# Kernel optimization log

Measured on AMD Instinct MI355X. Metric: run time of the kernel, lower is better.

## Reference

```python
import jax, jax.numpy as jnp
import numpy as np

# dims
M = 64      # memory_num -> T after attention pooling
B = 16
T = 2048    # input sequence length
C = 1024    # dim
H = 16      # attention heads
G = 2       # groups
V = 320     # num_vars
VQ = 1024   # vq_dim
D = VQ // G # var_dim = 512
TAU = 2.0   # curr_temp = max_temp at step 0


def setup_inputs() -> dict:
    key = jax.random.key(0)
    ks = jax.random.split(key, 16)
    s = 1.0 / np.sqrt(C)
    x = jax.random.normal(ks[0], (T, B, C), jnp.float32)
    padding_mask = jnp.zeros((B, T), bool)
    memory = jax.random.uniform(ks[1], (M, 1, C), jnp.float32)
    Wq = jax.random.normal(ks[2], (C, C), jnp.float32) * s
    Wk = jax.random.normal(ks[3], (C, C), jnp.float32) * s
    Wv = jax.random.normal(ks[4], (C, C), jnp.float32) * s
    Wo = jax.random.normal(ks[5], (C, C), jnp.float32) * s
    bq = jnp.zeros((C,), jnp.float32)
    bk = jnp.zeros((C,), jnp.float32)
    bv = jnp.zeros((C,), jnp.float32)
    bo = jnp.zeros((C,), jnp.float32)
    Wp = jax.random.normal(ks[6], (G * V, C), jnp.float32) * s
    bp = jnp.zeros((G * V,), jnp.float32)
    codebook = jax.random.uniform(ks[7], (1, G * V, D), jnp.float32)
    u = jax.random.uniform(ks[8], (B * M, G * V), jnp.float32, 1e-6, 1.0 - 1e-6)
    gumbel = -jnp.log(-jnp.log(u))
    return {"x": x, "padding_mask": padding_mask, "gumbel": gumbel,
            "memory": memory, "Wq": Wq, "bq": bq, "Wk": Wk, "bk": bk,
            "Wv": Wv, "bv": bv, "Wo": Wo, "bo": bo, "Wp": Wp, "bp": bp,
            "codebook": codebook}


def reference(x, padding_mask, gumbel, memory, Wq, bq, Wk, bk, Wv, bv, Wo, bo, Wp, bp, codebook):
    hd = C // H
    scale = hd ** -0.5
    # --- memory attention: queries are M learned memory slots, keys/values = x ---
    q = jnp.broadcast_to(memory, (M, B, C))              # repeat(1, B, 1)
    q = (q @ Wq.T + bq) * scale                          # [M,B,C]
    k = x @ Wk.T + bk                                    # [T,B,C]
    v = x @ Wv.T + bv
    split = lambda t: t.reshape(t.shape[0], B, H, hd).transpose(1, 2, 0, 3)  # [B,H,len,hd]
    qh, kh, vh = split(q), split(k), split(v)
    scores = jnp.einsum('bhqd,bhkd->bhqk', qh, kh)       # [B,H,M,T]
    neg = jnp.finfo(scores.dtype).min
    scores = jnp.where(padding_mask[:, None, None, :], neg, scores)
    attn = jax.nn.softmax(scores, axis=-1)
    ctx = jnp.einsum('bhqk,bhkd->bhqd', attn, vh)        # [B,H,M,hd]
    ctx = ctx.transpose(2, 0, 1, 3).reshape(M, B, C)
    h = ctx @ Wo.T + bo                                  # [M,B,C]
    # --- vector quantization (gumbel-softmax, hard=True, straight-through) ---
    h = h.transpose(1, 0, 2).reshape(B * M, C)           # [BT, C]
    logits = h @ Wp.T + bp                               # [BT, G*V]
    lg = logits.reshape(B * M * G, V)
    y = jax.nn.softmax((lg + gumbel.reshape(B * M * G, V)) / TAU, axis=-1)
    hard = jax.nn.one_hot(jnp.argmax(y, axis=-1), V, dtype=y.dtype)
    st = hard + y - jax.lax.stop_gradient(y)             # straight-through one-hot
    sel = st.reshape(B * M, G, V)
    code = codebook.reshape(G, V, D)
    # onehot-multiply-sum expressed as contraction (same math, no [BT,G*V,D] blowup)
    out = jnp.einsum('ngv,gvd->ngd', sel, code).reshape(B, M, G * D)
    out = out.transpose(1, 0, 2)                         # [T_mem, B, vq_dim]
    vq_logits = jax.nn.softmax(logits.reshape(B * M, G, V), axis=-1)
    return out, vq_logits
```

## Files before the change

### kernel.cpp

```cpp
#include <hip/hip_runtime.h>
#include <hip/hip_bf16.h>
#include <cstdint>
#include <cstddef>

#define TM 2048
#define BB 16
#define CC 1024
#define HH 16
#define HD 64
#define MM 64
#define GG 2
#define VV 320
#define DD 512

typedef __attribute__((ext_vector_type(4))) float f32x4;
typedef __attribute__((ext_vector_type(8))) short s16x8;
typedef __attribute__((ext_vector_type(8))) unsigned short u16x8;
typedef __attribute__((ext_vector_type(4))) unsigned int u32x4;

#define SW4(r) ((((r) & 3) ^ (((r) >> 2) & 3)))

#define GLL16(gp, lp) __builtin_amdgcn_global_load_lds( \
    (const __attribute__((address_space(1))) unsigned int*)(gp), \
    (__attribute__((address_space(3))) unsigned int*)(lp), 16, 0, 0)

static __device__ __forceinline__ unsigned short bf16_rne(float f) {
    unsigned u = __builtin_bit_cast(unsigned, f);
    u += 0x7FFFu + ((u >> 16) & 1u);
    return (unsigned short)(u >> 16);
}
static __device__ __forceinline__ float bf16_f32(unsigned short b) {
    return __builtin_bit_cast(float, (unsigned)b << 16);
}

__global__ void wsplit_swz(const float* __restrict__ W,
                           unsigned short* __restrict__ hi,
                           unsigned short* __restrict__ lo, int ngroups) {
    int gidx = blockIdx.x * 256 + threadIdx.x;
    if (gidx >= ngroups) return;
    int row = gidx >> 7;
    int sl  = gidx & 127;
    int k   = sl * 8;
    int slot = (k >> 3) & 3;
    int kp = (k & ~31) | (((slot ^ SW4(row & 15)) & 3) << 3);
    const float* src = W + (size_t)row * 1024 + k;
    f32x4 a = *(const f32x4*)src;
    f32x4 b = *(const f32x4*)(src + 4);
    u16x8 h, l;
    #pragma unroll
    for (int e = 0; e < 4; ++e) {
        unsigned short hh = bf16_rne(a[e]); h[e] = hh; l[e] = bf16_rne(a[e] - bf16_f32(hh));
        unsigned short hh2 = bf16_rne(b[e]); h[4 + e] = hh2; l[4 + e] = bf16_rne(b[e] - bf16_f32(hh2));
    }
    *(u16x8*)(hi + (size_t)row * 1024 + kp) = h;
    *(u16x8*)(lo + (size_t)row * 1024 + kp) = l;
}

__global__ __launch_bounds__(256) void gemm_f32_64(
    const float* __restrict__ A, const float* __restrict__ W,
    const float* __restrict__ bias, float* __restrict__ C,
    int K, int N, float alpha)
{
    __shared__ float At[64][17];
    __shared__ float Wt[64][17];
    const int tid = threadIdx.x;
    const int tx = tid & 15, ty = tid >> 4;
    const int n0 = blockIdx.x * 64, r0 = blockIdx.y * 64;
    const int srow = tid >> 2, skc = (tid & 3) * 4;

    float acc[4][4] = {};
    const float* ap = A + (size_t)(r0 + srow) * K + skc;
    const float* wp = W + (size_t)(n0 + srow) * K + skc;

    for (int k0 = 0; k0 < K; k0 += 16) {
        f32x4 av = *(const f32x4*)(ap + k0);
        f32x4 wv = *(const f32x4*)(wp + k0);
        __syncthreads();
        #pragma unroll
        for (int e = 0; e < 4; ++e) { At[srow][skc + e] = av[e]; Wt[srow][skc + e] = wv[e]; }
        __syncthreads();
        #pragma unroll
        for (int k = 0; k < 16; ++k) {
            float a[4], b[4];
            #pragma unroll
            for (int i = 0; i < 4; ++i) a[i] = At[ty + 16 * i][k];
            #pragma unroll
            for (int j = 0; j < 4; ++j) b[j] = Wt[tx + 16 * j][k];
            #pragma unroll
            for (int i = 0; i < 4; ++i)
                #pragma unroll
                for (int j = 0; j < 4; ++j)
                    acc[i][j] += a[i] * b[j];
        }
    }
    float bv[4];
    #pragma unroll
    for (int j = 0; j < 4; ++j) bv[j] = bias[n0 + tx + 16 * j];
    #pragma unroll
    for (int i = 0; i < 4; ++i)
        #pragma unroll
        for (int j = 0; j < 4; ++j)
            C[(size_t)(r0 + ty + 16 * i) * N + (n0 + tx + 16 * j)] = (acc[i][j] + bv[j]) * alpha;
}

__global__ __launch_bounds__(256) void kv_gemm3(
    const unsigned short* __restrict__ Xh, const unsigned short* __restrict__ Xl,
    const unsigned short* __restrict__ WKh, const unsigned short* __restrict__ WKl,
    const unsigned short* __restrict__ WVh, const unsigned short* __restrict__ WVl,
    const float* __restrict__ biasK, const float* __restrict__ biasV,
    unsigned short* __restrict__ outK, unsigned short* __restrict__ outV)
{
    const unsigned short* Wh; const unsigned short* Wl; const float* bias; unsigned short* out;
    if (blockIdx.z == 0) { Wh = WKh; Wl = WKl; bias = biasK; out = outK; }
    else                 { Wh = WVh; Wl = WVl; bias = biasV; out = outV; }

    const int rb = blockIdx.x * 32 + (blockIdx.y >> 3);
    const int cb = blockIdx.y & 7;
    const int r0 = rb * 128, n0 = cb * 128;

    __shared__ unsigned short Ah[128 * 32];
    __shared__ unsigned short Al[128 * 32];
    __shared__ unsigned short Bh[128 * 32];
    __shared__ unsigned short Bl[128 * 32];

    const int tid = threadIdx.x;
    const int lane = tid & 63;
    const int w = tid >> 6;
    const int wr = w >> 1, wc = w & 1;
    const int l15 = lane & 15;
    const int g = lane >> 4;
    const int lrow = lane >> 2;
    const int lslot = lane & 3;
    const int w32 = w * 32;

    f32x4 acc[4][4];
    #pragma unroll
    for (int i = 0; i < 4; ++i)
        #pragma unroll
        for (int j = 0; j < 4; ++j) acc[i][j] = f32x4{0.f, 0.f, 0.f, 0.f};

    for (int k0 = 0; k0 < CC; k0 += 32) {
        __syncthreads();
        #pragma unroll
        for (int i = 0; i < 2; ++i) {
            const int rs = w32 + i * 16;
            const size_t ga = (size_t)(r0 + rs + lrow) * CC + k0 + lslot * 8;
            const size_t gb = (size_t)(n0 + rs + lrow) * CC + k0 + lslot * 8;
            GLL16(Xh + ga, &Ah[rs * 32]);
            GLL16(Xl + ga, &Al[rs * 32]);
            GLL16(Wh + gb, &Bh[rs * 32]);
            GLL16(Wl + gb, &Bl[rs * 32]);
        }
        __syncthreads();

        s16x8 bhf[4], blf[4];
        #pragma unroll
        for (int ni = 0; ni < 4; ++ni) {
            int col = wc * 64 + ni * 16 + l15;
            int off = col * 32 + (((g ^ SW4(col & 15)) & 3) << 3);
            bhf[ni] = *(const s16x8*)&Bh[off];
            blf[ni] = *(const s16x8*)&Bl[off];
        }
        #pragma unroll
        for (int mi = 0; mi < 4; ++mi) {
            int row = wr * 64 + mi * 16 + l15;
            int off = row * 32 + (((g ^ SW4(row & 15)) & 3) << 3);
            s16x8 ah = *(const s16x8*)&Ah[off];
            s16x8 al = *(const s16x8*)&Al[off];
            #pragma unroll
            for (int ni = 0; ni < 4; ++ni) {
                acc[mi][ni] = __builtin_amdgcn_mfma_f32_16x16x32_bf16(ah, bhf[ni], acc[mi][ni], 0, 0, 0);
                acc[mi][ni] = __builtin_amdgcn_mfma_f32_16x16x32_bf16(al, bhf[ni], acc[mi][ni], 0, 0, 0);
                acc[mi][ni] = __builtin_amdgcn_mfma_f32_16x16x32_bf16(ah, blf[ni], acc[mi][ni], 0, 0, 0);
            }
        }
    }

    #pragma unroll
    for (int ni = 0; ni < 4; ++ni) {
        int col = n0 + wc * 64 + ni * 16 + l15;
        float bv = bias[col];
        int hh = col >> 6, d = col & 63;
        #pragma unroll
        for (int mi = 0; mi < 4; ++mi) {
            #pragma unroll
            for (int j = 0; j < 4; ++j) {
                int r = r0 + wr * 64 + mi * 16 + g * 4 + j;
                int t = r >> 4, bb = r & 15;
                size_t base = ((size_t)(bb * HH + hh) * TM + t) * 128;
                float val = acc[mi][ni][j] + bv;
                unsigned short hi = bf16_rne(val);
                out[base + d] = hi;
                out[base + 64 + d] = bf16_rne(val - bf16_f32(hi));
            }
        }
    }
}

__global__ __launch_bounds__(256) void kv_gemm2(
    const float* __restrict__ X,
    const unsigned short* __restrict__ WKh, const unsigned short* __restrict__ WKl,
    const unsigned short* __restrict__ WVh, const unsigned short* __restrict__ WVl,
    const float* __restrict__ biasK, const float* __restrict__ biasV,
    unsigned short* __restrict__ outK, unsigned short* __restrict__ outV)
{
    const unsigned short* Wh; const unsigned short* Wl; const float* bias; unsigned short* out;
    if (blockIdx.z == 0) { Wh = WKh; Wl = WKl; bias = biasK; out = outK; }
    else                 { Wh = WVh; Wl = WVl; bias = biasV; out = outV; }

    const int rb = blockIdx.x * 32 + (blockIdx.y >> 3);
    const int cb = blockIdx.y & 7;
    const int r0 = rb * 128, n0 = cb * 128;

    __shared__ unsigned short Ah[128 * 32];
    __shared__ unsigned short Al[128 * 32];
    __shared__ unsigned short Bh[128 * 32];
    __shared__ unsigned short Bl[128 * 32];

    const int tid = threadIdx.x;
    const int lane = tid & 63;
    const int wid = tid >> 6;
    const int wr = wid >> 1, wc = wid & 1;
    const int l15 = lane & 15;
    const int g = lane >> 4;

    f32x4 acc[4][4];
    #pragma unroll
    for (int i = 0; i < 4; ++i)
        #pragma unroll
        for (int j = 0; j < 4; ++j) acc[i][j] = f32x4{0.f, 0.f, 0.f, 0.f};

    for (int k0 = 0; k0 < CC; k0 += 32) {
        f32x4 xa[2][2]; u16x8 wbh[2], wbl[2];
        int rowc[2], slotc[2];
        #pragma unroll
        for (int c = 0; c < 2; ++c) {
            int g2 = tid + 256 * c;
            int row = g2 >> 2, slot = g2 & 3;
            rowc[c] = row; slotc[c] = slot;
            const float* xp = X + (size_t)(r0 + row) * CC + k0 + slot * 8;
            xa[c][0] = *(const f32x4*)xp;
            xa[c][1] = *(const f32x4*)(xp + 4);
            wbh[c] = *(const u16x8*)(Wh + (size_t)(n0 + row) * CC + k0 + slot * 8);
            wbl[c] = *(const u16x8*)(Wl + (size_t)(n0 + row) * CC + k0 + slot * 8);
        }
        __syncthreads();
        #pragma unroll
        for (int c = 0; c < 2; ++c) {
            int row = rowc[c], slot = slotc[c];
// ... 316 lines not shown
                unsigned g0 = __shfl(pkl[2 * ks][0], srcB), g1 = __shfl(pkl[2 * ks + 1][0], srcB);
                tl[2] = hsel ? g1 : g0;
                unsigned h0 = __shfl(pkl[2 * ks][1], srcB), h1 = __shfl(pkl[2 * ks + 1][1], srcB);
                tl[3] = hsel ? h1 : h0;
            }
            Ph[ks] = __builtin_bit_cast(s16x8, th);
            Pl[ks] = __builtin_bit_cast(s16x8, tl);
        }

        #pragma unroll
        for (int mt = 0; mt < 4; ++mt) {
            int dr = mt * 16 + l15;
            #pragma unroll
            for (int ks = 0; ks < 2; ++ks) {
                int spb = ((ks * 4 + g) ^ (dr & 7)) & 7;
                s16x8 vh = *(const s16x8*)&Vt[buf][dr * 128 + spb * 8];
                s16x8 vl = *(const s16x8*)&Vt[buf][dr * 128 + (8 + spb) * 8];
                O[mt] = __builtin_amdgcn_mfma_f32_16x16x32_bf16(vh, Ph[ks], O[mt], 0, 0, 0);
                O[mt] = __builtin_amdgcn_mfma_f32_16x16x32_bf16(vl, Ph[ks], O[mt], 0, 0, 0);
                O[mt] = __builtin_amdgcn_mfma_f32_16x16x32_bf16(vh, Pl[ks], O[mt], 0, 0, 0);
            }
        }

        __syncthreads();
        if (ch + 1 < NCH) { WRITE_LDS(buf ^ 1); }
        __syncthreads();
    }

    const int qg = w * 16 + l15;
    if (SPLIT == 1) {
        float inv = 1.0f / l_run;
        #pragma unroll
        for (int mt = 0; mt < 4; ++mt)
            #pragma unroll
            for (int j = 0; j < 4; ++j) {
                int d = mt * 16 + g * 4 + j;
                ctx_or_pO[(size_t)(b * MM + qg) * CC + h * 64 + d] = O[mt][j] * inv;
            }
    } else {
        float* po = ctx_or_pO + (size_t)bid * 4096;
        #pragma unroll
        for (int mt = 0; mt < 4; ++mt)
            #pragma unroll
            for (int j = 0; j < 4; ++j) {
                int d = mt * 16 + g * 4 + j;
                po[d * 64 + qg] = O[mt][j];
            }
        if (g == 0) { partM[bid * 64 + qg] = m_run; partL[bid * 64 + qg] = l_run; }
    }
    #undef ISSUE_LOADS
    #undef WRITE_LDS
}

__global__ __launch_bounds__(256) void attn_merge(
    const float* __restrict__ pO, const float* __restrict__ pM,
    const float* __restrict__ pL, float* __restrict__ ctx)
{
    const int bh = blockIdx.x, b = bh >> 4, h = bh & 15, tid = threadIdx.x;
    __shared__ float w0s[64], w1s[64], invs[64];
    if (tid < 64) {
        float m0 = pM[(bh * 2) * 64 + tid], m1 = pM[(bh * 2 + 1) * 64 + tid];
        float l0 = pL[(bh * 2) * 64 + tid], l1 = pL[(bh * 2 + 1) * 64 + tid];
        float M = fmaxf(m0, m1);
        float w0 = expf(m0 - M), w1 = expf(m1 - M);
        w0s[tid] = w0; w1s[tid] = w1;
        invs[tid] = 1.0f / (l0 * w0 + l1 * w1);
    }
    __syncthreads();
    const float* o0 = pO + (size_t)(bh * 2) * 4096;
    const float* o1 = pO + (size_t)(bh * 2 + 1) * 4096;
    #pragma unroll
    for (int i = 0; i < 16; ++i) {
        int e = tid + 256 * i;
        int q = e >> 6, d = e & 63;
        float v = o0[d * 64 + q] * w0s[q] + o1[d * 64 + q] * w1s[q];
        ctx[(size_t)(b * MM + q) * CC + h * 64 + d] = v * invs[q];
    }
}

__global__ __launch_bounds__(256) void finalize_kernel(
    const float* __restrict__ logits, const float* __restrict__ gumbel,
    const float* __restrict__ codebook, float* __restrict__ out)
{
    __shared__ float lrow[GG * VV];
    __shared__ float red[256];
    __shared__ int redi[256];
    __shared__ int sel[GG];

    const int n = blockIdx.x, tid = threadIdx.x;
    const size_t OUT1 = (size_t)MM * BB * GG * DD;

    for (int e = tid; e < GG * VV; e += 256) lrow[e] = logits[(size_t)n * GG * VV + e];
    __syncthreads();

    for (int g = 0; g < GG; ++g) {
        float bvv = -3.0e38f; int bii = 0x7FFFFFFF;
        for (int j = tid; j < VV; j += 256) {
            float z = lrow[g * VV + j] + gumbel[(size_t)n * GG * VV + g * VV + j];
            if (z > bvv) { bvv = z; bii = j; }
        }
        red[tid] = bvv; redi[tid] = bii;
        __syncthreads();
        for (int s = 128; s > 0; s >>= 1) {
            if (tid < s) {
                float ov = red[tid + s]; int oi = redi[tid + s];
                if (ov > red[tid] || (ov == red[tid] && oi < redi[tid])) { red[tid] = ov; redi[tid] = oi; }
            }
            __syncthreads();
        }
        if (tid == 0) sel[g] = redi[0];
        __syncthreads();

        float mx = -3.0e38f;
        for (int j = tid; j < VV; j += 256) mx = fmaxf(mx, lrow[g * VV + j]);
        red[tid] = mx;
        __syncthreads();
        for (int s = 128; s > 0; s >>= 1) {
            if (tid < s) red[tid] = fmaxf(red[tid], red[tid + s]);
            __syncthreads();
        }
        float rmax = red[0];
        __syncthreads();
        float sm = 0.f;
        for (int j = tid; j < VV; j += 256) sm += expf(lrow[g * VV + j] - rmax);
        red[tid] = sm;
        __syncthreads();
        for (int s = 128; s > 0; s >>= 1) {
            if (tid < s) red[tid] += red[tid + s];
            __syncthreads();
// ... 8 lines not shown
    const int b = n >> 6, m = n & 63;
    const size_t ob = ((size_t)m * BB + b) * (GG * DD);
    for (int g = 0; g < GG; ++g) {
        const float* cb = codebook + ((size_t)g * VV + sel[g]) * DD;
        for (int d = tid; d < DD; d += 256) out[ob + g * DD + d] = cb[d];
    }
}

extern "C" void kernel_launch(void* const* d_in, const int* in_sizes, int n_in,
                              void* d_out, int out_size, void* d_ws, size_t ws_size,
                              hipStream_t stream)
{
    const float* x        = (const float*)d_in[0];
    const float* gumbel   = (const float*)d_in[2];
    const float* memory   = (const float*)d_in[3];
    const float* Wq       = (const float*)d_in[4];
    const float* bq       = (const float*)d_in[5];
    const float* Wk       = (const float*)d_in[6];
    const float* bk       = (const float*)d_in[7];
    const float* Wv       = (const float*)d_in[8];
    const float* bv       = (const float*)d_in[9];
    const float* Wo       = (const float*)d_in[10];
    const float* bo       = (const float*)d_in[11];
    const float* Wp       = (const float*)d_in[12];
    const float* bp       = (const float*)d_in[13];
    const float* codebook = (const float*)d_in[14];
    float* out = (float*)d_out;

    char* ws = (char*)d_ws;
    size_t off = 0;
    auto take = [&](size_t bytes) -> void* {
        void* p = ws + off;
        off = (off + bytes + 255) & ~(size_t)255;
        return p;
    };

    float* q_ws   = (float*)take((size_t)MM * CC * 4);
    float* ctx_ws = (float*)take((size_t)BB * MM * CC * 4);
    float* lg_ws  = (float*)take((size_t)BB * MM * GG * VV * 4);
    unsigned short* wkh = (unsigned short*)take((size_t)CC * CC * 2);
    unsigned short* wkl = (unsigned short*)take((size_t)CC * CC * 2);
    unsigned short* wvh = (unsigned short*)take((size_t)CC * CC * 2);
    unsigned short* wvl = (unsigned short*)take((size_t)CC * CC * 2);
    unsigned short* k_ws = (unsigned short*)take((size_t)BB * HH * TM * 128 * 2);
    unsigned short* v_ws = (unsigned short*)take((size_t)BB * HH * TM * 128 * 2);

    const size_t XROWS = (size_t)TM * BB;
    const size_t xplane = XROWS * CC * 2;
    const size_t extra_need = 2 * (size_t)CC * CC * 2
                            + 2 * (size_t)GG * VV * CC * 2
                            + 2 * xplane + (1u << 20);
    const bool newpath = (ws_size >= off + extra_need);

    {
        int ngroups = CC * (CC / 8);
        wsplit_swz<<<dim3((ngroups + 255) / 256), 256, 0, stream>>>(Wk, wkh, wkl, ngroups);
        wsplit_swz<<<dim3((ngroups + 255) / 256), 256, 0, stream>>>(Wv, wvh, wvl, ngroups);
    }
    gemm_f32_64<<<dim3(CC / 64, MM / 64), 256, 0, stream>>>(memory, Wq, bq, q_ws, CC, CC, 0.125f);

    if (newpath) {
        unsigned short* woh = (unsigned short*)take((size_t)CC * CC * 2);
        unsigned short* wol = (unsigned short*)take((size_t)CC * CC * 2);
        unsigned short* wph = (unsigned short*)take((size_t)GG * VV * CC * 2);
        unsigned short* wpl = (unsigned short*)take((size_t)GG * VV * CC * 2);
        unsigned short* xh  = (unsigned short*)take(xplane);
        unsigned short* xl  = (unsigned short*)take(xplane);

        char* xr = (char*)xh;
        size_t xo = 0;
        auto xtake = [&](size_t bytes) -> void* {
            void* p = xr + xo;
            xo = (xo + bytes + 255) & ~(size_t)255;
            return p;
        };
        float* pO = (float*)xtake((size_t)512 * 4096 * 4);
        float* pM = (float*)xtake((size_t)512 * 64 * 4);
        float* pL = (float*)xtake((size_t)512 * 64 * 4);
        unsigned short* cth = (unsigned short*)xtake((size_t)BB * MM * CC * 2);
        unsigned short* ctl = (unsigned short*)xtake((size_t)BB * MM * CC * 2);
        unsigned short* hh  = (unsigned short*)xtake((size_t)BB * MM * CC * 2);
        unsigned short* hl  = (unsigned short*)xtake((size_t)BB * MM * CC * 2);

        {
            int ngroups = CC * (CC / 8);
            wsplit_swz<<<dim3((ngroups + 255) / 256), 256, 0, stream>>>(Wo, woh, wol, ngroups);
            int ngp = GG * VV * (CC / 8);
            wsplit_swz<<<dim3((ngp + 255) / 256), 256, 0, stream>>>(Wp, wph, wpl, ngp);
            int ngx = (int)(XROWS * (CC / 8));
            wsplit_swz<<<dim3((ngx + 255) / 256), 256, 0, stream>>>(x, xh, xl, ngx);
        }

        kv_gemm3<<<dim3(8, 256, 2), 256, 0, stream>>>(xh, xl, wkh, wkl, wvh, wvl, bk, bv, k_ws, v_ws);

        attn2<2><<<dim3(512), 256, 0, stream>>>(q_ws, k_ws, v_ws, pO, pM, pL);
        attn_merge<<<dim3(256), 256, 0, stream>>>(pO, pM, pL, ctx_ws);

        {
            int ngc = BB * MM * (CC / 8);
            wsplit_swz<<<dim3((ngc + 255) / 256), 256, 0, stream>>>(ctx_ws, cth, ctl, ngc);
        }
        mfma_gemm3<1><<<dim3(CC / 128, (BB * MM) / 128), 256, 0, stream>>>(
            cth, ctl, woh, wol, bo, CC, nullptr, hh, hl);
        mfma_gemm3<0><<<dim3((GG * VV) / 128, (BB * MM) / 128), 256, 0, stream>>>(
            hh, hl, wph, wpl, bp, GG * VV, lg_ws, nullptr, nullptr);
    } else {
        float* h_ws = (float*)take((size_t)BB * MM * CC * 4);
        const size_t part_bytes = (size_t)512 * 4096 * 4 + 2 * (size_t)512 * 64 * 4 + 4096;
        const bool split2 = (ws_size >= off + part_bytes);

        kv_gemm2<<<dim3(8, 256, 2), 256, 0, stream>>>(x, wkh, wkl, wvh, wvl, bk, bv, k_ws, v_ws);

        if (split2) {
            float* pO = (float*)take((size_t)512 * 4096 * 4);
            float* pM = (float*)take((size_t)512 * 64 * 4);
            float* pL = (float*)take((size_t)512 * 64 * 4);
            attn2<2><<<dim3(512), 256, 0, stream>>>(q_ws, k_ws, v_ws, pO, pM, pL);
            attn_merge<<<dim3(256), 256, 0, stream>>>(pO, pM, pL, ctx_ws);
        } else {
            attn2<1><<<dim3(256), 256, 0, stream>>>(q_ws, k_ws, v_ws, ctx_ws, nullptr, nullptr);
        }

        gemm_f32_64<<<dim3(CC / 64, (BB * MM) / 64), 256, 0, stream>>>(ctx_ws, Wo, bo, h_ws, CC, CC, 1.0f);
        gemm_f32_64<<<dim3((GG * VV) / 64, (BB * MM) / 64), 256, 0, stream>>>(h_ws, Wp, bp, lg_ws, CC, GG * VV, 1.0f);
    }

    finalize_kernel<<<dim3(BB * MM), 256, 0, stream>>>(lg_ws, gumbel, codebook, out);
}
```

Measured before the change: 802.2 us.

## Rework K/V projection GEMM with 512 threads, triple-buffered LDS and staged epilogue

Replaces the K/V projection GEMM with a 512-thread variant. Each of the 8 warps now covers a 64x32 sub-tile, and the single-buffer global-to-LDS loop becomes a 3-stage pipeline with explicit vmcnt waits and raised MFMA priority, so loads overlap compute. The epilogue writes the bf16 hi/lo outputs through a swizzled LDS tile and then stores 16-byte vectors, replacing scattered 2-byte global stores. This uses three times the LDS (96KB), which can reduce occupancy, and fewer accumulators per warp means more LDS reads per MFMA.

```diff
diff --git a/kernel.cpp b/kernel.cpp
--- a/kernel.cpp
+++ b/kernel.cpp
@@ -103,7 +103,7 @@
             C[(size_t)(r0 + ty + 16 * i) * N + (n0 + tx + 16 * j)] = (acc[i][j] + bv[j]) * alpha;
 }
 
-__global__ __launch_bounds__(256) void kv_gemm3(
+__global__ __launch_bounds__(512) void kv_gemm4(
     const unsigned short* __restrict__ Xh, const unsigned short* __restrict__ Xl,
     const unsigned short* __restrict__ WKh, const unsigned short* __restrict__ WKl,
     const unsigned short* __restrict__ WVh, const unsigned short* __restrict__ WVl,
@@ -118,81 +118,126 @@
     const int cb = blockIdx.y & 7;
     const int r0 = rb * 128, n0 = cb * 128;
 
-    __shared__ unsigned short Ah[128 * 32];
-    __shared__ unsigned short Al[128 * 32];
-    __shared__ unsigned short Bh[128 * 32];
-    __shared__ unsigned short Bl[128 * 32];
+    __shared__ unsigned short L[3][4][128 * 32];
 
     const int tid = threadIdx.x;
     const int lane = tid & 63;
     const int w = tid >> 6;
-    const int wr = w >> 1, wc = w & 1;
+    const int wr = w >> 2, wc = w & 3;
     const int l15 = lane & 15;
     const int g = lane >> 4;
-    const int lrow = lane >> 2;
-    const int lslot = lane & 3;
-    const int w32 = w * 32;
-
-    f32x4 acc[4][4];
+    const int srow = tid >> 2;
+    const int sslot = tid & 3;
+    const int w512 = w * 512;
+
+    const size_t gaBase = (size_t)(r0 + srow) * CC + sslot * 8;
+    const size_t gbBase = (size_t)(n0 + srow) * CC + sslot * 8;
+
+    #define STAGE4(buf, k0)                                   \
+        {                                                     \
+            GLL16(Xh + gaBase + (k0), &L[buf][0][w512]);      \
+            GLL16(Xl + gaBase + (k0), &L[buf][1][w512]);      \
+            GLL16(Wh + gbBase + (k0), &L[buf][2][w512]);      \
+            GLL16(Wl + gbBase + (k0), &L[buf][3][w512]);      \
+        }
+
+    f32x4 acc[4][2];
     #pragma unroll
     for (int i = 0; i < 4; ++i)
         #pragma unroll
-        for (int j = 0; j < 4; ++j) acc[i][j] = f32x4{0.f, 0.f, 0.f, 0.f};
-
-    for (int k0 = 0; k0 < CC; k0 += 32) {
-        __syncthreads();
-        #pragma unroll
-        for (int i = 0; i < 2; ++i) {
-            const int rs = w32 + i * 16;
-            const size_t ga = (size_t)(r0 + rs + lrow) * CC + k0 + lslot * 8;
-            const size_t gb = (size_t)(n0 + rs + lrow) * CC + k0 + lslot * 8;
-            GLL16(Xh + ga, &Ah[rs * 32]);
-            GLL16(Xl + ga, &Al[rs * 32]);
-            GLL16(Wh + gb, &Bh[rs * 32]);
-            GLL16(Wl + gb, &Bl[rs * 32]);
-        }
-        __syncthreads();
-
-        s16x8 bhf[4], blf[4];
-        #pragma unroll
-        for (int ni = 0; ni < 4; ++ni) {
-            int col = wc * 64 + ni * 16 + l15;
-            int off = col * 32 + (((g ^ SW4(col & 15)) & 3) << 3);
-            bhf[ni] = *(const s16x8*)&Bh[off];
-            blf[ni] = *(const s16x8*)&Bl[off];
-        }
+        for (int j = 0; j < 2; ++j) acc[i][j] = f32x4{0.f, 0.f, 0.f, 0.f};
+
+    int aoff[4], boff[2];
+    #pragma unroll
+    for (int mi = 0; mi < 4; ++mi) {
+        int row = wr * 64 + mi * 16 + l15;
+        aoff[mi] = row * 32 + (((g ^ SW4(row & 15)) & 3) << 3);
+    }
+    #pragma unroll
+    for (int ni = 0; ni < 2; ++ni) {
+        int col = wc * 32 + ni * 16 + l15;
+        boff[ni] = col * 32 + (((g ^ SW4(col & 15)) & 3) << 3);
+    }
+
+    STAGE4(0, 0);
+    STAGE4(1, 32);
+    asm volatile("s_waitcnt vmcnt(4)" ::: "memory");
+    __builtin_amdgcn_s_barrier();
+
+    const int NT = 32;
+    for (int t = 0; t < NT; ++t) {
+        const int buf = t % 3;
+        if (t + 2 < NT) {
+            const int stg = (t + 2) % 3;
+            STAGE4(stg, (t + 2) * 32);
+        }
+
+        s16x8 bhf[2], blf[2];
+        #pragma unroll
+        for (int ni = 0; ni < 2; ++ni) {
+            bhf[ni] = *(const s16x8*)&L[buf][2][boff[ni]];
+            blf[ni] = *(const s16x8*)&L[buf][3][boff[ni]];
+        }
+        s16x8 ah[4], al[4];
         #pragma unroll
         for (int mi = 0; mi < 4; ++mi) {
-            int row = wr * 64 + mi * 16 + l15;
-            int off = row * 32 + (((g ^ SW4(row & 15)) & 3) << 3);
-            s16x8 ah = *(const s16x8*)&Ah[off];
-            s16x8 al = *(const s16x8*)&Al[off];
-            #pragma unroll
-            for (int ni = 0; ni < 4; ++ni) {
-                acc[mi][ni] = __builtin_amdgcn_mfma_f32_16x16x32_bf16(ah, bhf[ni], acc[mi][ni], 0, 0, 0);
-                acc[mi][ni] = __builtin_amdgcn_mfma_f32_16x16x32_bf16(al, bhf[ni], acc[mi][ni], 0, 0, 0);
-                acc[mi][ni] = __builtin_amdgcn_mfma_f32_16x16x32_bf16(ah, blf[ni], acc[mi][ni], 0, 0, 0);
-            }
-        }
-    }
-
-    #pragma unroll
-    for (int ni = 0; ni < 4; ++ni) {
-        int col = n0 + wc * 64 + ni * 16 + l15;
-        float bv = bias[col];
-        int hh = col >> 6, d = col & 63;
+            ah[mi] = *(const s16x8*)&L[buf][0][aoff[mi]];
+            al[mi] = *(const s16x8*)&L[buf][1][aoff[mi]];
+        }
+
+        __builtin_amdgcn_s_setprio(1);
         #pragma unroll
         for (int mi = 0; mi < 4; ++mi) {
             #pragma unroll
+            for (int ni = 0; ni < 2; ++ni) {
+                acc[mi][ni] = __builtin_amdgcn_mfma_f32_16x16x32_bf16(ah[mi], bhf[ni], acc[mi][ni], 0, 0, 0);
+                acc[mi][ni] = __builtin_amdgcn_mfma_f32_16x16x32_bf16(al[mi], bhf[ni], acc[mi][ni], 0, 0, 0);
+                acc[mi][ni] = __builtin_amdgcn_mfma_f32_16x16x32_bf16(ah[mi], blf[ni], acc[mi][ni], 0, 0, 0);
+            }
+        }
+        __builtin_amdgcn_s_setprio(0);
+
+        if (t + 2 < NT) {
+            asm volatile("s_waitcnt vmcnt(4)" ::: "memory");
+        } else if (t + 1 < NT) {
+            asm volatile("s_waitcnt vmcnt(0)" ::: "memory");
+        }
+        __builtin_amdgcn_s_barrier();
+    }
+    #undef STAGE4
+
+    __syncthreads();
+    unsigned short* OutL = &L[0][0][0];
+    #pragma unroll
+    for (int ni = 0; ni < 2; ++ni) {
+        const int cl = wc * 32 + ni * 16 + l15;
+        const float bv = bias[n0 + cl];
+        const int hsel = cl >> 6, d = cl & 63;
+        const int qh = (hsel << 4) + (d >> 3), ql = qh + 8;
+        #pragma unroll
+        for (int mi = 0; mi < 4; ++mi) {
+            #pragma unroll
             for (int j = 0; j < 4; ++j) {
-                int r = r0 + wr * 64 + mi * 16 + g * 4 + j;
-                int t = r >> 4, bb = r & 15;
-                size_t base = ((size_t)(bb * HH + hh) * TM + t) * 128;
+                const int rl = wr * 64 + mi * 16 + g * 4 + j;
                 float val = acc[mi][ni][j] + bv;
                 unsigned short hi = bf16_rne(val);
-                out[base + d] = hi;
-                out[base + 64 + d] = bf16_rne(val - bf16_f32(hi));
-            }
+                OutL[rl * 256 + ((qh ^ (rl & 31)) << 3) + (d & 7)] = hi;
+                OutL[rl * 256 + ((ql ^ (rl & 31)) << 3) + (d & 7)] = bf16_rne(val - bf16_f32(hi));
+            }
+        }
+    }
+    __syncthreads();
+    {
+        const int r = tid >> 2;
+        const int hsel2 = (tid >> 1) & 1, c2 = tid & 1;
+        const int rg = r0 + r;
+        const int tt = rg >> 4, bb2 = rg & 15;
+        const int hh2 = (n0 >> 6) + hsel2;
+        unsigned short* dst = out + ((size_t)(bb2 * HH + hh2) * TM + tt) * 128 + c2 * 64;
+        #pragma unroll
+        for (int i2 = 0; i2 < 8; ++i2) {
+            const int q = (hsel2 << 4) + (c2 << 3) + i2;
+            *(u16x8*)(dst + i2 * 8) = *(const u16x8*)&OutL[r * 256 + ((q ^ (r & 31)) << 3)];
         }
     }
 }
@@ -793,7 +838,7 @@
             wsplit_swz<<<dim3((ngx + 255) / 256), 256, 0, stream>>>(x, xh, xl, ngx);
         }
 
-        kv_gemm3<<<dim3(8, 256, 2), 256, 0, stream>>>(xh, xl, wkh, wkl, wvh, wvl, bk, bv, k_ws, v_ws);
+        kv_gemm4<<<dim3(8, 256, 2), 512, 0, stream>>>(xh, xl, wkh, wkl, wvh, wvl, bk, bv, k_ws, v_ws);
 
         attn2<2><<<dim3(512), 256, 0, stream>>>(q_ws, k_ws, v_ws, pO, pM, pL);
         attn_merge<<<dim3(256), 256, 0, stream>>>(pO, pM, pL, ctx_ws);
```

After: 843.8 us. 5.2% more time.

## Replace K/V projection GEMM with 256x256-tile pipelined 512-thread MFMA kernel

Applied to the files above, without the earlier changes.

Replaces the 128x128-tile split-bf16 K/V GEMM with a 256x256-tile kernel of 8 waves. It double-buffers 64-wide K slabs loaded directly into LDS with an 8-way XOR swizzle, and treats the three hi/lo product terms as 48 sequential K tiles. It uses XCD-aware block mapping, s_setprio around MFMA bursts, and manual vmcnt waits. The epilogue stages results through LDS so the scattered per-head K/V stores become coalesced 16-byte writes. The aim is higher MFMA utilisation and less global traffic per FLOP, at the cost of one block per CU, many barriers, and fragile hand-tuned synchronisation.

```diff
diff --git a/kernel.cpp b/kernel.cpp
--- a/kernel.cpp
+++ b/kernel.cpp
@@ -39,10 +39,31 @@
     int gidx = blockIdx.x * 256 + threadIdx.x;
     if (gidx >= ngroups) return;
     int row = gidx >> 7;
-    int sl  = gidx & 127;
-    int k   = sl * 8;
+    int k   = (gidx & 127) * 8;
     int slot = (k >> 3) & 3;
     int kp = (k & ~31) | (((slot ^ SW4(row & 15)) & 3) << 3);
+    const float* src = W + (size_t)row * 1024 + k;
+    f32x4 a = *(const f32x4*)src;
+    f32x4 b = *(const f32x4*)(src + 4);
+    u16x8 h, l;
+    #pragma unroll
+    for (int e = 0; e < 4; ++e) {
+        unsigned short hh = bf16_rne(a[e]); h[e] = hh; l[e] = bf16_rne(a[e] - bf16_f32(hh));
+        unsigned short hh2 = bf16_rne(b[e]); h[4 + e] = hh2; l[4 + e] = bf16_rne(b[e] - bf16_f32(hh2));
+    }
+    *(u16x8*)(hi + (size_t)row * 1024 + kp) = h;
+    *(u16x8*)(lo + (size_t)row * 1024 + kp) = l;
+}
+
+__global__ void wsplit_swz8(const float* __restrict__ W,
+                            unsigned short* __restrict__ hi,
+                            unsigned short* __restrict__ lo, int ngroups) {
+    int gidx = blockIdx.x * 256 + threadIdx.x;
+    if (gidx >= ngroups) return;
+    int row = gidx >> 7;
+    int k   = (gidx & 127) * 8;
+    int slot = (k >> 3) & 7;
+    int kp = (k & ~63) | (((slot ^ (row & 7)) & 7) << 3);
     const float* src = W + (size_t)row * 1024 + k;
     f32x4 a = *(const f32x4*)src;
     f32x4 b = *(const f32x4*)(src + 4);
@@ -103,98 +124,165 @@
             C[(size_t)(r0 + ty + 16 * i) * N + (n0 + tx + 16 * j)] = (acc[i][j] + bv[j]) * alpha;
 }
 
-__global__ __launch_bounds__(256) void kv_gemm3(
+__global__ __launch_bounds__(512, 1) void kv_gemm8(
     const unsigned short* __restrict__ Xh, const unsigned short* __restrict__ Xl,
     const unsigned short* __restrict__ WKh, const unsigned short* __restrict__ WKl,
     const unsigned short* __restrict__ WVh, const unsigned short* __restrict__ WVl,
     const float* __restrict__ biasK, const float* __restrict__ biasV,
     unsigned short* __restrict__ outK, unsigned short* __restrict__ outV)
 {
-    const unsigned short* Wh; const unsigned short* Wl; const float* bias; unsigned short* out;
-    if (blockIdx.z == 0) { Wh = WKh; Wl = WKl; bias = biasK; out = outK; }
-    else                 { Wh = WVh; Wl = WVl; bias = biasV; out = outV; }
-
-    const int rb = blockIdx.x * 32 + (blockIdx.y >> 3);
-    const int cb = blockIdx.y & 7;
-    const int r0 = rb * 128, n0 = cb * 128;
-
-    __shared__ unsigned short Ah[128 * 32];
-    __shared__ unsigned short Al[128 * 32];
-    __shared__ unsigned short Bh[128 * 32];
-    __shared__ unsigned short Bl[128 * 32];
-
-    const int tid = threadIdx.x;
-    const int lane = tid & 63;
-    const int w = tid >> 6;
-    const int wr = w >> 1, wc = w & 1;
-    const int l15 = lane & 15;
-    const int g = lane >> 4;
-    const int lrow = lane >> 2;
-    const int lslot = lane & 3;
-    const int w32 = w * 32;
-
-    f32x4 acc[4][4];
-    #pragma unroll
-    for (int i = 0; i < 4; ++i)
-        #pragma unroll
-        for (int j = 0; j < 4; ++j) acc[i][j] = f32x4{0.f, 0.f, 0.f, 0.f};
-
-    for (int k0 = 0; k0 < CC; k0 += 32) {
-        __syncthreads();
-        #pragma unroll
-        for (int i = 0; i < 2; ++i) {
-            const int rs = w32 + i * 16;
-            const size_t ga = (size_t)(r0 + rs + lrow) * CC + k0 + lslot * 8;
-            const size_t gb = (size_t)(n0 + rs + lrow) * CC + k0 + lslot * 8;
-            GLL16(Xh + ga, &Ah[rs * 32]);
-            GLL16(Xl + ga, &Al[rs * 32]);
-            GLL16(Wh + gb, &Bh[rs * 32]);
-            GLL16(Wl + gb, &Bl[rs * 32]);
-        }
-        __syncthreads();
-
-        s16x8 bhf[4], blf[4];
-        #pragma unroll
-        for (int ni = 0; ni < 4; ++ni) {
-            int col = wc * 64 + ni * 16 + l15;
-            int off = col * 32 + (((g ^ SW4(col & 15)) & 3) << 3);
-            bhf[ni] = *(const s16x8*)&Bh[off];
-            blf[ni] = *(const s16x8*)&Bl[off];
-        }
-        #pragma unroll
-        for (int mi = 0; mi < 4; ++mi) {
-            int row = wr * 64 + mi * 16 + l15;
-            int off = row * 32 + (((g ^ SW4(row & 15)) & 3) << 3);
-            s16x8 ah = *(const s16x8*)&Ah[off];
-            s16x8 al = *(const s16x8*)&Al[off];
+    const int bid = blockIdx.x;
+    const int xcd = bid & 7, i = bid >> 3;
+    const int mb = xcd * 16 + (i >> 3);
+    const int j = i & 7, z = j >> 2, nb = j & 3;
+
+    const unsigned short *Bh_g, *Bl_g; const float* bias; unsigned short* out;
+    if (z == 0) { Bh_g = WKh; Bl_g = WKl; bias = biasK; out = outK; }
+    else        { Bh_g = WVh; Bl_g = WVl; bias = biasV; out = outV; }
+    const int r0 = mb * 256, n0 = nb * 256;
+
+    __shared__ __align__(16) unsigned short L[65536];
+
+    const int tid = threadIdx.x, lane = tid & 63, w = tid >> 6;
+    const int wr = w >> 2, wc = w & 3;
+    const int l15 = lane & 15, g = lane >> 4;
+
+    f32x4 acc[8][4];
+    #pragma unroll
+    for (int mi = 0; mi < 8; ++mi)
+        #pragma unroll
+        for (int ni = 0; ni < 4; ++ni) acc[mi][ni] = f32x4{0.f, 0.f, 0.f, 0.f};
+
+    auto STAGE_A = [&](int buf, int tau) {
+        const int k0in = (tau & 15) * 64;
+        const unsigned short* P = ((tau >> 4) == 1) ? Xl : Xh;
+        #pragma unroll
+        for (int half = 0; half < 2; ++half)
+            #pragma unroll
+            for (int ii = 0; ii < 2; ++ii) {
+                const int e0 = ii * 512 + w * 64;
+                const int e = e0 + lane;
+                const unsigned short* src = P + (size_t)(r0 + half * 128 + (e >> 3)) * 1024
+                                              + k0in + (e & 7) * 8;
+                GLL16(src, &L[(buf * 2 + half) * 8192 + e0 * 8]);
+            }
+    };
+    auto STAGE_B = [&](int buf, int tau) {
+        const int k0in = (tau & 15) * 64;
+        const unsigned short* P = ((tau >> 4) == 2) ? Bl_g : Bh_g;
+        #pragma unroll
+        for (int half = 0; half < 2; ++half)
+            #pragma unroll
+            for (int ii = 0; ii < 2; ++ii) {
+                const int e0 = ii * 512 + w * 64;
+                const int e = e0 + lane;
+                const unsigned short* src = P + (size_t)(n0 + half * 128 + (e >> 3)) * 1024
+                                              + k0in + (e & 7) * 8;
+                GLL16(src, &L[32768 + (buf * 2 + half) * 8192 + e0 * 8]);
+            }
+    };
+
+    s16x8 a_[8], b_[2];
+    #define RD_A(BUF, KS) { _Pragma("unroll")                                        \
+        for (int mi = 0; mi < 8; ++mi) {                                             \
+            int row = mi * 16 + l15;                                                 \
+            a_[mi] = *(const s16x8*)&L[((BUF) * 2 + wr) * 8192 + row * 64            \
+                                       + ((((KS) * 4 + g) ^ (l15 & 7)) << 3)]; } }
+    #define RD_B(BUF, KS, NF0) { _Pragma("unroll")                                   \
+        for (int q = 0; q < 2; ++q) {                                                \
+            int row = (wc & 1) * 64 + ((NF0) + q) * 16 + l15;                        \
+            b_[q] = *(const s16x8*)&L[32768 + ((BUF) * 2 + (wc >> 1)) * 8192         \
+                                      + row * 64 + ((((KS) * 4 + g) ^ (l15 & 7)) << 3)]; } }
+    #define MFMA16(NF0) { _Pragma("unroll")                                          \
+        for (int mi = 0; mi < 8; ++mi) {                                             \
+            acc[mi][NF0]     = __builtin_amdgcn_mfma_f32_16x16x32_bf16(a_[mi], b_[0], acc[mi][NF0], 0, 0, 0);     \
+            acc[mi][NF0 + 1] = __builtin_amdgcn_mfma_f32_16x16x32_bf16(a_[mi], b_[1], acc[mi][NF0 + 1], 0, 0, 0); } }
+    #define FENCE asm volatile("" ::: "memory")
+    #define BAR   __builtin_amdgcn_s_barrier()
+    #define PRIO1 __builtin_amdgcn_s_setprio(1)
+    #define PRIO0 __builtin_amdgcn_s_setprio(0)
+
+    const int NT = 48;
+
+    STAGE_A(0, 0);
+    STAGE_B(0, 0);
+    STAGE_A(1, 1);
+    FENCE;
+    asm volatile("s_waitcnt vmcnt(4)" ::: "memory");
+    BAR;
+
+    #define KTILE(BUF, TAU) {                                                        \
+                                     \
+        RD_A(BUF, 0); RD_B(BUF, 0, 0);                                               \
+        if ((TAU) + 1 < NT) STAGE_B((BUF) ^ 1, (TAU) + 1);                           \
+        FENCE; BAR; PRIO1; MFMA16(0); PRIO0; FENCE; BAR;                             \
+                                    \
+        RD_B(BUF, 0, 2);                                                             \
+        FENCE; BAR; PRIO1; MFMA16(2); PRIO0; FENCE; BAR;                             \
+                                                    \
+        RD_A(BUF, 1); RD_B(BUF, 1, 0);                                               \
+        FENCE; BAR; PRIO1; MFMA16(0); PRIO0; FENCE; BAR;                             \
+                        \
+        RD_B(BUF, 1, 2);                                                             \
+        if ((TAU) + 2 < NT) STAGE_A(BUF, (TAU) + 2);                                 \
+        FENCE; BAR; PRIO1; MFMA16(2); PRIO0;                                         \
+        if ((TAU) + 2 < NT) { asm volatile("s_waitcnt vmcnt(4)" ::: "memory"); }     \
+        else                { asm volatile("s_waitcnt vmcnt(0)" ::: "memory"); }     \
+        FENCE; BAR; }
+
+    #pragma unroll 1
+    for (int t2 = 0; t2 < NT / 2; ++t2) {
+        KTILE(0, 2 * t2);
+        KTILE(1, 2 * t2 + 1);
+    }
+    #undef KTILE
+    #undef RD_A
+    #undef RD_B
+    #undef MFMA16
+
+    const int hh4 = n0 >> 6;
+    #pragma unroll 1
+    for (int pass = 0; pass < 2; ++pass) {
+        __syncthreads();
+        if (wr == pass) {
             #pragma unroll
             for (int ni = 0; ni < 4; ++ni) {
-                acc[mi][ni] = __builtin_amdgcn_mfma_f32_16x16x32_bf16(ah, bhf[ni], acc[mi][ni], 0, 0, 0);
-                acc[mi][ni] = __builtin_amdgcn_mfma_f32_16x16x32_bf16(al, bhf[ni], acc[mi][ni], 0, 0, 0);
-                acc[mi][ni] = __builtin_amdgcn_mfma_f32_16x16x32_bf16(ah, blf[ni], acc[mi][ni], 0, 0, 0);
-            }
-        }
-    }
-
-    #pragma unroll
-    for (int ni = 0; ni < 4; ++ni) {
-        int col = n0 + wc * 64 + ni * 16 + l15;
-        float bv = bias[col];
-        int hh = col >> 6, d = col & 63;
-        #pragma unroll
-        for (int mi = 0; mi < 4; ++mi) {
-            #pragma unroll
-            for (int j = 0; j < 4; ++j) {
-                int r = r0 + wr * 64 + mi * 16 + g * 4 + j;
-                int t = r >> 4, bb = r & 15;
-                size_t base = ((size_t)(bb * HH + hh) * TM + t) * 128;
-                float val = acc[mi][ni][j] + bv;
-                unsigned short hi = bf16_rne(val);
-                out[base + d] = hi;
-                out[base + 64 + d] = bf16_rne(val - bf16_f32(hi));
-            }
-        }
-    }
+                const int d = ni * 16 + l15;
+                const float bv = bias[n0 + wc * 64 + d];
+                #pragma unroll
+                for (int mi = 0; mi < 8; ++mi) {
+                    #pragma unroll
+                    for (int jj = 0; jj < 4; ++jj) {
+                        const int row = mi * 16 + g * 4 + jj;
+                        const int key = (row & 7) ^ (wc << 1);
+                        const int sl = (((d >> 3) ^ key) & 7) << 3;
+                        float val = acc[mi][ni][jj] + bv;
+                        unsigned short hi = bf16_rne(val);
+                        L[row * 512 + wc * 128 + sl + (d & 7)] = hi;
+                        L[row * 512 + wc * 128 + 64 + sl + (d & 7)] = bf16_rne(val - bf16_f32(hi));
+                    }
+                }
+            }
+        }
+        __syncthreads();
+        {
+            const int rrow = tid >> 2, hh = tid & 3;
+            const int rg = r0 + pass * 128 + rrow;
+            const int tt = rg >> 4, bb = rg & 15;
+            unsigned short* dst = out + ((size_t)(bb * HH + hh4 + hh) * TM + tt) * 128;
+            const int key = (rrow & 7) ^ (hh << 1);
+            #pragma unroll
+            for (int q = 0; q < 16; ++q) {
+                const int pl = q >> 3, dc = q & 7;
+                u16x8 v = *(const u16x8*)&L[rrow * 512 + hh * 128 + pl * 64 + ((dc ^ key) & 7) * 8];
+                *(u16x8*)(dst + q * 8) = v;
+            }
+        }
+    }
+    #undef FENCE
+    #undef BAR
+    #undef PRIO1
+    #undef PRIO0
 }
 
 __global__ __launch_bounds__(256) void kv_gemm2(
@@ -754,11 +842,6 @@
                             + 2 * xplane + (1u << 20);
     const bool newpath = (ws_size >= off + extra_need);
 
-    {
-        int ngroups = CC * (CC / 8);
-        wsplit_swz<<<dim3((ngroups + 255) / 256), 256, 0, stream>>>(Wk, wkh, wkl, ngroups);
-        wsplit_swz<<<dim3((ngroups + 255) / 256), 256, 0, stream>>>(Wv, wvh, wvl, ngroups);
-    }
     gemm_f32_64<<<dim3(CC / 64, MM / 64), 256, 0, stream>>>(memory, Wq, bq, q_ws, CC, CC, 0.125f);
 
     if (newpath) {
@@ -786,14 +869,16 @@
 
         {
             int ngroups = CC * (CC / 8);
+            wsplit_swz8<<<dim3((ngroups + 255) / 256), 256, 0, stream>>>(Wk, wkh, wkl, ngroups);
+            wsplit_swz8<<<dim3((ngroups + 255) / 256), 256, 0, stream>>>(Wv, wvh, wvl, ngroups);
             wsplit_swz<<<dim3((ngroups + 255) / 256), 256, 0, stream>>>(Wo, woh, wol, ngroups);
             int ngp = GG * VV * (CC / 8);
             wsplit_swz<<<dim3((ngp + 255) / 256), 256, 0, stream>>>(Wp, wph, wpl, ngp);
             int ngx = (int)(XROWS * (CC / 8));
-            wsplit_swz<<<dim3((ngx + 255) / 256), 256, 0, stream>>>(x, xh, xl, ngx);
-        }
-
-        kv_gemm3<<<dim3(8, 256, 2), 256, 0, stream>>>(xh, xl, wkh, wkl, wvh, wvl, bk, bv, k_ws, v_ws);
+            wsplit_swz8<<<dim3((ngx + 255) / 256), 256, 0, stream>>>(x, xh, xl, ngx);
+        }
+
+        kv_gemm8<<<dim3(1024), 512, 0, stream>>>(xh, xl, wkh, wkl, wvh, wvl, bk, bv, k_ws, v_ws);
 
         attn2<2><<<dim3(512), 256, 0, stream>>>(q_ws, k_ws, v_ws, pO, pM, pL);
         attn_merge<<<dim3(256), 256, 0, stream>>>(pO, pM, pL, ctx_ws);
@@ -811,6 +896,12 @@
         const size_t part_bytes = (size_t)512 * 4096 * 4 + 2 * (size_t)512 * 64 * 4 + 4096;
         const bool split2 = (ws_size >= off + part_bytes);
 
+        {
+            int ngroups = CC * (CC / 8);
+            wsplit_swz<<<dim3((ngroups + 255) / 256), 256, 0, stream>>>(Wk, wkh, wkl, ngroups);
+            wsplit_swz<<<dim3((ngroups + 255) / 256), 256, 0, stream>>>(Wv, wvh, wvl, ngroups);
+        }
+
         kv_gemm2<<<dim3(8, 256, 2), 256, 0, stream>>>(x, wkh, wkl, wvh, wvl, bk, bv, k_ws, v_ws);
 
         if (split2) {
```

Result: slower. 849.1 us (+5.8%).

## Double-buffer kv GEMM, stage epilogue via LDS, fuse split kernels and merge

Applied to the files above, without the earlier changes.

The K/V projection GEMM now double-buffers its LDS tiles, overlapping the next tile's global-to-LDS loads with the current tile's MFMAs. It also raises wave priority during the MFMA section and writes output through LDS so the global stores are coalesced 16-byte rows. The five bf16 hi/lo split launches become one fused kernel, and the ctx split is folded into the attention-merge kernel, removing launches and a round trip through fp32 ctx. LDS use per block doubles, which may lower occupancy.

```diff
diff --git a/kernel.cpp b/kernel.cpp
--- a/kernel.cpp
+++ b/kernel.cpp
@@ -33,14 +33,12 @@
     return __builtin_bit_cast(float, (unsigned)b << 16);
 }
 
-__global__ void wsplit_swz(const float* __restrict__ W,
-                           unsigned short* __restrict__ hi,
-                           unsigned short* __restrict__ lo, int ngroups) {
-    int gidx = blockIdx.x * 256 + threadIdx.x;
-    if (gidx >= ngroups) return;
+static __device__ __forceinline__ void wsplit_one(
+    const float* __restrict__ W, unsigned short* __restrict__ hi,
+    unsigned short* __restrict__ lo, int gidx)
+{
     int row = gidx >> 7;
-    int sl  = gidx & 127;
-    int k   = sl * 8;
+    int k   = (gidx & 127) * 8;
     int slot = (k >> 3) & 3;
     int kp = (k & ~31) | (((slot ^ SW4(row & 15)) & 3) << 3);
     const float* src = W + (size_t)row * 1024 + k;
@@ -56,6 +54,35 @@
     *(u16x8*)(lo + (size_t)row * 1024 + kp) = l;
 }
 
+__global__ void wsplit_swz(const float* __restrict__ W,
+                           unsigned short* __restrict__ hi,
+                           unsigned short* __restrict__ lo, int ngroups) {
+    int gidx = blockIdx.x * 256 + threadIdx.x;
+    if (gidx < ngroups) wsplit_one(W, hi, lo, gidx);
+}
+
+#define NG_W  131072
+#define NG_P  81920
+#define NG_X  4194304
+__global__ void wsplit_fused(
+    const float* __restrict__ Wk, unsigned short* __restrict__ wkh, unsigned short* __restrict__ wkl,
+    const float* __restrict__ Wv, unsigned short* __restrict__ wvh, unsigned short* __restrict__ wvl,
+    const float* __restrict__ Wo, unsigned short* __restrict__ woh, unsigned short* __restrict__ wol,
+    const float* __restrict__ Wp, unsigned short* __restrict__ wph, unsigned short* __restrict__ wpl,
+    const float* __restrict__ X,  unsigned short* __restrict__ xh,  unsigned short* __restrict__ xl)
+{
+    int gidx = blockIdx.x * 256 + threadIdx.x;
+    if (gidx < NG_X) { wsplit_one(X, xh, xl, gidx); return; }
+    gidx -= NG_X;
+    if (gidx < NG_W) { wsplit_one(Wk, wkh, wkl, gidx); return; }
+    gidx -= NG_W;
+    if (gidx < NG_W) { wsplit_one(Wv, wvh, wvl, gidx); return; }
+    gidx -= NG_W;
+    if (gidx < NG_W) { wsplit_one(Wo, woh, wol, gidx); return; }
+    gidx -= NG_W;
+    if (gidx < NG_P) { wsplit_one(Wp, wph, wpl, gidx); }
+}
+
 __global__ __launch_bounds__(256) void gemm_f32_64(
     const float* __restrict__ A, const float* __restrict__ W,
     const float* __restrict__ bias, float* __restrict__ C,
@@ -103,7 +130,7 @@
             C[(size_t)(r0 + ty + 16 * i) * N + (n0 + tx + 16 * j)] = (acc[i][j] + bv[j]) * alpha;
 }
 
-__global__ __launch_bounds__(256) void kv_gemm3(
+__global__ __launch_bounds__(256) void kv_gemm5(
     const unsigned short* __restrict__ Xh, const unsigned short* __restrict__ Xl,
     const unsigned short* __restrict__ WKh, const unsigned short* __restrict__ WKl,
     const unsigned short* __restrict__ WVh, const unsigned short* __restrict__ WVl,
@@ -118,10 +145,7 @@
     const int cb = blockIdx.y & 7;
     const int r0 = rb * 128, n0 = cb * 128;
 
-    __shared__ unsigned short Ah[128 * 32];
-    __shared__ unsigned short Al[128 * 32];
-    __shared__ unsigned short Bh[128 * 32];
-    __shared__ unsigned short Bl[128 * 32];
+    __shared__ __align__(16) unsigned short L[2][4][128 * 32];
 
     const int tid = threadIdx.x;
     const int lane = tid & 63;
@@ -139,34 +163,52 @@
         #pragma unroll
         for (int j = 0; j < 4; ++j) acc[i][j] = f32x4{0.f, 0.f, 0.f, 0.f};
 
-    for (int k0 = 0; k0 < CC; k0 += 32) {
-        __syncthreads();
+    int aoff[4], boff[4];
+    #pragma unroll
+    for (int mi = 0; mi < 4; ++mi) {
+        int row = wr * 64 + mi * 16 + l15;
+        aoff[mi] = row * 32 + (((g ^ SW4(row & 15)) & 3) << 3);
+    }
+    #pragma unroll
+    for (int ni = 0; ni < 4; ++ni) {
+        int col = wc * 64 + ni * 16 + l15;
+        boff[ni] = col * 32 + (((g ^ SW4(col & 15)) & 3) << 3);
+    }
+
+    auto STAGE = [&](int buf, int k0) {
         #pragma unroll
         for (int i = 0; i < 2; ++i) {
             const int rs = w32 + i * 16;
             const size_t ga = (size_t)(r0 + rs + lrow) * CC + k0 + lslot * 8;
             const size_t gb = (size_t)(n0 + rs + lrow) * CC + k0 + lslot * 8;
-            GLL16(Xh + ga, &Ah[rs * 32]);
-            GLL16(Xl + ga, &Al[rs * 32]);
-            GLL16(Wh + gb, &Bh[rs * 32]);
-            GLL16(Wl + gb, &Bl[rs * 32]);
-        }
-        __syncthreads();
+            GLL16(Xh + ga, &L[buf][0][rs * 32]);
+            GLL16(Xl + ga, &L[buf][1][rs * 32]);
+            GLL16(Wh + gb, &L[buf][2][rs * 32]);
+            GLL16(Wl + gb, &L[buf][3][rs * 32]);
+        }
+    };
+
+    STAGE(0, 0);
+    asm volatile("s_waitcnt vmcnt(0)" ::: "memory");
+    __builtin_amdgcn_s_barrier();
+
+    const int NT = 32;
+    #pragma unroll 1
+    for (int t = 0; t < NT; ++t) {
+        const int buf = t & 1;
+        if (t + 1 < NT) STAGE(buf ^ 1, (t + 1) * 32);
 
         s16x8 bhf[4], blf[4];
         #pragma unroll
         for (int ni = 0; ni < 4; ++ni) {
-            int col = wc * 64 + ni * 16 + l15;
-            int off = col * 32 + (((g ^ SW4(col & 15)) & 3) << 3);
-            bhf[ni] = *(const s16x8*)&Bh[off];
-            blf[ni] = *(const s16x8*)&Bl[off];
-        }
+            bhf[ni] = *(const s16x8*)&L[buf][2][boff[ni]];
+            blf[ni] = *(const s16x8*)&L[buf][3][boff[ni]];
+        }
+        __builtin_amdgcn_s_setprio(1);
         #pragma unroll
         for (int mi = 0; mi < 4; ++mi) {
-            int row = wr * 64 + mi * 16 + l15;
-            int off = row * 32 + (((g ^ SW4(row & 15)) & 3) << 3);
-            s16x8 ah = *(const s16x8*)&Ah[off];
-            s16x8 al = *(const s16x8*)&Al[off];
+            s16x8 ah = *(const s16x8*)&L[buf][0][aoff[mi]];
+            s16x8 al = *(const s16x8*)&L[buf][1][aoff[mi]];
             #pragma unroll
             for (int ni = 0; ni < 4; ++ni) {
                 acc[mi][ni] = __builtin_amdgcn_mfma_f32_16x16x32_bf16(ah, bhf[ni], acc[mi][ni], 0, 0, 0);
@@ -174,25 +216,43 @@
                 acc[mi][ni] = __builtin_amdgcn_mfma_f32_16x16x32_bf16(ah, blf[ni], acc[mi][ni], 0, 0, 0);
             }
         }
-    }
-
+        __builtin_amdgcn_s_setprio(0);
+
+        asm volatile("s_waitcnt vmcnt(0)" ::: "memory");
+        __builtin_amdgcn_s_barrier();
+    }
+
+    unsigned short* OutL = &L[0][0][0];
+    __syncthreads();
     #pragma unroll
     for (int ni = 0; ni < 4; ++ni) {
-        int col = n0 + wc * 64 + ni * 16 + l15;
-        float bv = bias[col];
-        int hh = col >> 6, d = col & 63;
+        const int cl = wc * 64 + ni * 16 + l15;
+        const float bv = bias[n0 + cl];
+        const int hsel = cl >> 6, d = cl & 63;
+        const int qh = (hsel << 4) + (d >> 3), ql = qh + 8;
         #pragma unroll
         for (int mi = 0; mi < 4; ++mi) {
             #pragma unroll
             for (int j = 0; j < 4; ++j) {
-                int r = r0 + wr * 64 + mi * 16 + g * 4 + j;
-                int t = r >> 4, bb = r & 15;
-                size_t base = ((size_t)(bb * HH + hh) * TM + t) * 128;
+                const int rl = wr * 64 + mi * 16 + g * 4 + j;
                 float val = acc[mi][ni][j] + bv;
                 unsigned short hi = bf16_rne(val);
-                out[base + d] = hi;
-                out[base + 64 + d] = bf16_rne(val - bf16_f32(hi));
-            }
+                OutL[rl * 256 + ((qh ^ (rl & 31)) << 3) + (d & 7)] = hi;
+                OutL[rl * 256 + ((ql ^ (rl & 31)) << 3) + (d & 7)] = bf16_rne(val - bf16_f32(hi));
+            }
+        }
+    }
+    __syncthreads();
+    {
+        const int r2 = tid >> 1, hsel2 = tid & 1;
+        const int rg = r0 + r2;
+        const int tt = rg >> 4, bb = rg & 15;
+        const int head = (n0 >> 6) + hsel2;
+        unsigned short* dst = out + ((size_t)(bb * HH + head) * TM + tt) * 128;
+        #pragma unroll
+        for (int q = 0; q < 16; ++q) {
+            const int slot = (hsel2 << 4) + q;
+            *(u16x8*)(dst + q * 8) = *(const u16x8*)&OutL[r2 * 256 + ((slot ^ (r2 & 31)) << 3)];
         }
     }
 }
@@ -617,9 +677,10 @@
     #undef WRITE_LDS
 }
 
-__global__ __launch_bounds__(256) void attn_merge(
+__global__ __launch_bounds__(256) void attn_merge2(
     const float* __restrict__ pO, const float* __restrict__ pM,
-    const float* __restrict__ pL, float* __restrict__ ctx)
+    const float* __restrict__ pL,
+    unsigned short* __restrict__ cth, unsigned short* __restrict__ ctl)
 {
     const int bh = blockIdx.x, b = bh >> 4, h = bh & 15, tid = threadIdx.x;
     __shared__ float w0s[64], w1s[64], invs[64];
@@ -638,8 +699,14 @@
     for (int i = 0; i < 16; ++i) {
         int e = tid + 256 * i;
         int q = e >> 6, d = e & 63;
-        float v = o0[d * 64 + q] * w0s[q] + o1[d * 64 + q] * w1s[q];
-        ctx[(size_t)(b * MM + q) * CC + h * 64 + d] = v * invs[q];
+        float v = (o0[d * 64 + q] * w0s[q] + o1[d * 64 + q] * w1s[q]) * invs[q];
+        int n = b * MM + q;
+        int c = h * 64 + d;
+        int slot = (c >> 3) & 3;
+        int kp = (c & ~31) | (((slot ^ SW4(n & 15)) & 3) << 3) | (c & 7);
+        unsigned short hi = bf16_rne(v);
+        cth[(size_t)n * 1024 + kp] = hi;
+        ctl[(size_t)n * 1024 + kp] = bf16_rne(v - bf16_f32(hi));
     }
 }
 
@@ -754,11 +821,6 @@
                             + 2 * xplane + (1u << 20);
     const bool newpath = (ws_size >= off + extra_need);
 
-    {
-        int ngroups = CC * (CC / 8);
-        wsplit_swz<<<dim3((ngroups + 255) / 256), 256, 0, stream>>>(Wk, wkh, wkl, ngroups);
-        wsplit_swz<<<dim3((ngroups + 255) / 256), 256, 0, stream>>>(Wv, wvh, wvl, ngroups);
-    }
     gemm_f32_64<<<dim3(CC / 64, MM / 64), 256, 0, stream>>>(memory, Wq, bq, q_ws, CC, CC, 0.125f);
 
     if (newpath) {
@@ -785,23 +847,17 @@
         unsigned short* hl  = (unsigned short*)xtake((size_t)BB * MM * CC * 2);
 
         {
-            int ngroups = CC * (CC / 8);
-            wsplit_swz<<<dim3((ngroups + 255) / 256), 256, 0, stream>>>(Wo, woh, wol, ngroups);
-            int ngp = GG * VV * (CC / 8);
-            wsplit_swz<<<dim3((ngp + 255) / 256), 256, 0, stream>>>(Wp, wph, wpl, ngp);
-            int ngx = (int)(XROWS * (CC / 8));
-            wsplit_swz<<<dim3((ngx + 255) / 256), 256, 0, stream>>>(x, xh, xl, ngx);
-        }
-
-        kv_gemm3<<<dim3(8, 256, 2), 256, 0, stream>>>(xh, xl, wkh, wkl, wvh, wvl, bk, bv, k_ws, v_ws);
+            const int total = NG_X + 3 * NG_W + NG_P;
+            wsplit_fused<<<dim3((total + 255) / 256), 256, 0, stream>>>(
+                Wk, wkh, wkl, Wv, wvh, wvl, Wo, woh, wol, Wp, wph, wpl, x, xh, xl);
+        }
+
+        kv_gemm5<<<dim3(8, 256, 2), 256, 0, stream>>>(
+            xh, xl, wkh, wkl, wvh, wvl, bk, bv, k_ws, v_ws);
 
         attn2<2><<<dim3(512), 256, 0, stream>>>(q_ws, k_ws, v_ws, pO, pM, pL);
-        attn_merge<<<dim3(256), 256, 0, stream>>>(pO, pM, pL, ctx_ws);
-
-        {
-            int ngc = BB * MM * (CC / 8);
-            wsplit_swz<<<dim3((ngc + 255) / 256), 256, 0, stream>>>(ctx_ws, cth, ctl, ngc);
-        }
+        attn_merge2<<<dim3(256), 256, 0, stream>>>(pO, pM, pL, cth, ctl);
+
         mfma_gemm3<1><<<dim3(CC / 128, (BB * MM) / 128), 256, 0, stream>>>(
             cth, ctl, woh, wol, bo, CC, nullptr, hh, hl);
         mfma_gemm3<0><<<dim3((GG * VV) / 128, (BB * MM) / 128), 256, 0, stream>>>(
@@ -811,6 +867,12 @@
         const size_t part_bytes = (size_t)512 * 4096 * 4 + 2 * (size_t)512 * 64 * 4 + 4096;
         const bool split2 = (ws_size >= off + part_bytes);
 
+        {
+            int ngroups = CC * (CC / 8);
+            wsplit_swz<<<dim3((ngroups + 255) / 256), 256, 0, stream>>>(Wk, wkh, wkl, ngroups);
+            wsplit_swz<<<dim3((ngroups + 255) / 256), 256, 0, stream>>>(Wv, wvh, wvl, ngroups);
+        }
+
         kv_gemm2<<<dim3(8, 256, 2), 256, 0, stream>>>(x, wkh, wkl, wvh, wvl, bk, bv, k_ws, v_ws);
 
         if (split2) {
@@ -818,7 +880,9 @@
             float* pM = (float*)take((size_t)512 * 64 * 4);
             float* pL = (float*)take((size_t)512 * 64 * 4);
             attn2<2><<<dim3(512), 256, 0, stream>>>(q_ws, k_ws, v_ws, pO, pM, pL);
-            attn_merge<<<dim3(256), 256, 0, stream>>>(pO, pM, pL, ctx_ws);
+            unsigned short* cth = nullptr; unsigned short* ctl = nullptr;
+            (void)cth; (void)ctl;
+            attn2<1><<<dim3(256), 256, 0, stream>>>(q_ws, k_ws, v_ws, ctx_ws, nullptr, nullptr);
         } else {
             attn2<1><<<dim3(256), 256, 0, stream>>>(q_ws, k_ws, v_ws, ctx_ws, nullptr, nullptr);
         }
```

Measured after the change: 754.9 us. -5.9%, faster.
